# Kernel optimization log

Measured on AMD Instinct MI355X. Metric: run time of the kernel, lower is better.

Reference implementation:

```python
import jax, jax.numpy as jnp
import numpy as np

H = 51  # hidden size hardcoded in the module

def _lstm_cell(x, h, c, W_ih, W_hh, b_ih, b_hh):
    # PyTorch LSTMCell: gates ordered (i, f, g, o)
    z = x @ W_ih.T + h @ W_hh.T + b_ih + b_hh  # [B, 4H]
    i, f, g, o = jnp.split(z, 4, axis=-1)
    i = jax.nn.sigmoid(i)
    f = jax.nn.sigmoid(f)
    g = jnp.tanh(g)
    o = jax.nn.sigmoid(o)
    c_new = f * c + i * g
    h_new = o * jnp.tanh(c_new)
    return h_new, c_new

def setup_inputs() -> dict:
    key = jax.random.key(0)
    ks = jax.random.split(key, 12)
    B, T = 512, 512
    s = 1.0 / np.sqrt(H)  # PyTorch default init scale
    def u(k, shape):
        return jax.random.uniform(k, shape, jnp.float32, -s, s)
    return {
        "input": jax.random.normal(ks[0], (B, T), jnp.float32),
        "W_ih1": u(ks[1], (4 * H, 1)),
        "W_hh1": u(ks[2], (4 * H, H)),
        "b_ih1": u(ks[3], (4 * H,)),
        "b_hh1": u(ks[4], (4 * H,)),
        "W_ih2": u(ks[5], (4 * H, H)),
        "W_hh2": u(ks[6], (4 * H, H)),
        "b_ih2": u(ks[7], (4 * H,)),
        "b_hh2": u(ks[8], (4 * H,)),
        "W_lin": u(ks[9], (1, H)),
        "b_lin": u(ks[10], (1,)),
        "future": 0,
    }

def reference(input, W_ih1, W_hh1, b_ih1, b_hh1, W_ih2, W_hh2, b_ih2, b_hh2, W_lin, b_lin, future):
    B, T = input.shape
    h1 = jnp.zeros((B, H), input.dtype)
    c1 = jnp.zeros((B, H), input.dtype)
    h2 = jnp.zeros((B, H), input.dtype)
    c2 = jnp.zeros((B, H), input.dtype)

    def step(carry, x_t):
        h1, c1, h2, c2 = carry
        h1, c1 = _lstm_cell(x_t, h1, c1, W_ih1, W_hh1, b_ih1, b_hh1)
        h2, c2 = _lstm_cell(h1, h2, c2, W_ih2, W_hh2, b_ih2, b_hh2)
        out = h2 @ W_lin.T + b_lin  # [B, 1]
        return (h1, c1, h2, c2), out

    xs = jnp.transpose(input)[:, :, None]  # [T, B, 1]
    carry, outs = jax.lax.scan(step, (h1, c1, h2, c2), xs)
    outputs = jnp.transpose(outs[:, :, 0])  # [B, T]

    if future > 0:
        last = outs[-1]  # [B, 1]

        def fstep(carry, _):
            state, x = carry
            state, out = step(state, x)
            return (state, out), out

        _, fouts = jax.lax.scan(fstep, (carry, last), None, length=future)
        outputs = jnp.concatenate([outputs, jnp.transpose(fouts[:, :, 0])], axis=1)
    return outputs
```

## Files before the change

kernel.cpp:

```cpp
#include <hip/hip_runtime.h>

#define Hh 51
#define TT 512
#define MR 2
#define NBLK 256
#define BT 512
#define SHR 80
#define NIT 514
#define LOG2E 1.4426950408889634f

typedef _Float16 half8 __attribute__((ext_vector_type(8)));
typedef __attribute__((ext_vector_type(4))) float f32x4;

__device__ __forceinline__ float fexp2(float x){ return __builtin_amdgcn_exp2f(x); }
__device__ __forceinline__ float frcp(float x){ return __builtin_amdgcn_rcpf(x); }
__device__ __forceinline__ unsigned short h16bits(_Float16 h){
    union { _Float16 h; unsigned short u; } c; c.h = h; return c.u;
}
__device__ __forceinline__ unsigned packhl(float v){
    _Float16 hi = (_Float16)v;
    _Float16 lo = (_Float16)(v - (float)hi);
    return (unsigned)h16bits(hi) | ((unsigned)h16bits(lo) << 16);
}

__device__ __forceinline__ float lstm_update(float vg0, float vg1, float vg2,
                                             float vg3, float& cst){
    float ei = fexp2(vg0), ef = fexp2(vg1), eg = fexp2(vg2), eo = fexp2(vg3);
    float ii = frcp(1.f + ei);
    float ff = frcp(1.f + ef);
    float gg = fmaf(-2.f, frcp(1.f + eg), 1.f);
    float oo = frcp(1.f + eo);
    cst = fmaf(ff, cst, ii * gg);
    float r  = frcp(1.f + fexp2(2.f * LOG2E * cst));
    return fmaf(-2.f * oo, r, oo);
}

#define MFMAH(a,b,c) __builtin_amdgcn_mfma_f32_16x16x32_f16(a,b,c,0,0,0)

__global__ __launch_bounds__(BT, 2) void lstm2_fold(
    const float* __restrict__ input,
    const float* __restrict__ W_ih1,
    const float* __restrict__ W_hh1,
    const float* __restrict__ b_ih1,
    const float* __restrict__ b_hh1,
    const float* __restrict__ W_ih2,
    const float* __restrict__ W_hh2,
    const float* __restrict__ b_ih2,
    const float* __restrict__ b_hh2,
    const float* __restrict__ W_lin,
    const float* __restrict__ b_lin,
    float* __restrict__ out)
{
    __shared__ unsigned xsp[(TT+1)*MR];
    __shared__ float ob[TT*MR];
    __shared__ __align__(16) _Float16 H1[2][16*SHR];
    __shared__ __align__(16) _Float16 H2[2][16*SHR];

    const int tid  = threadIdx.x;
    const int wv   = tid >> 6;
    const int lane = tid & 63;
    const int quad = lane >> 4;
    const int n16  = lane & 15;
    const int row0 = blockIdx.x * MR;
    const bool g1  = (wv < 4);
    const bool w3  = (wv == 3);
    const int  w   = g1 ? wv : (wv - 4);
    const int  l   = 13 * w + n16;
    const bool valid = (n16 <= 12) && (l < Hh);
    const bool liveA = ((n16 & 11) == 0);
    const bool updL  = (quad < MR) && valid;
    const bool xw    = (wv == 0) && (n16 == 0) && (quad < MR);
    const int  fo    = n16 * SHR + quad * 8;
    const int  ho    = (quad * 4) * SHR + l;

#pragma unroll
    for (int i = 0; i < MR; ++i) {
        int idx = i * BT + tid; int m = idx >> 9, t = idx & 511;
        xsp[t * MR + m] = packhl(input[(row0 + m) * TT + t]);
    }
    if (tid < MR) xsp[TT * MR + tid] = 0u;
    for (int i = tid; i < 2 * 16 * SHR / 2; i += BT) {
        ((int*)H1)[i] = 0; ((int*)H2)[i] = 0;
    }

    half8 z8 = {0,0,0,0,0,0,0,0};
    half8 B1[4][2];
    half8 B2[4][2], B3[4][2];
    half8 Bout[2];
    const f32x4 zc = (f32x4){0.f,0.f,0.f,0.f};
#pragma unroll
    for (int gt = 0; gt < 4; ++gt) {
        const float gs = (gt == 2) ? (2.f * LOG2E) : (-LOG2E);
        int jrow = gt * Hh + l;
        float bias = 0.f, wih = 0.f;
        if (valid) {
            bias = gs * (g1 ? (b_ih1[jrow] + b_hh1[jrow]) : (b_ih2[jrow] + b_hh2[jrow]));
            wih  = g1 ? (gs * W_ih1[jrow]) : 0.f;
        }
        _Float16 bhi = (_Float16)bias;
        _Float16 blo = (_Float16)(bias - (float)bhi);
        _Float16 wih_h = (_Float16)wih;
#pragma unroll
        for (int kt = 0; kt < 2; ++kt) {
            B1[gt][kt] = z8; B2[gt][kt] = z8; B3[gt][kt] = z8;
#pragma unroll
            for (int jj = 0; jj < 8; ++jj) {
                int k = kt * 32 + quad * 8 + jj;
                if (valid) {
                    if (g1) {
                        if (k < Hh)       B1[gt][kt][jj] = (_Float16)(gs * W_hh1[jrow * Hh + k]);
                        else if (k == 51) B1[gt][kt][jj] = bhi;
                        else if (k == 52 || k == 53) B1[gt][kt][jj] = wih_h;
                        else if (k == 54) B1[gt][kt][jj] = blo;
                    } else {
                        if (k < Hh) {
                            B2[gt][kt][jj] = (_Float16)(gs * W_ih2[jrow * Hh + k]);
                            B3[gt][kt][jj] = (_Float16)(gs * W_hh2[jrow * Hh + k]);
                        } else if (k == 51) B2[gt][kt][jj] = bhi;
                        else if (k == 54)   B2[gt][kt][jj] = blo;
                    }
                }
            }
        }
    }
    {
        float blf = b_lin[0];
        _Float16 blhi = (_Float16)blf;
        _Float16 bllo = (_Float16)(blf - (float)blhi);
#pragma unroll
        for (int kt = 0; kt < 2; ++kt) {
            Bout[kt] = z8;
#pragma unroll
            for (int jj = 0; jj < 8; ++jj) {
                int k = kt * 32 + quad * 8 + jj;
                if (w3 && n16 == 0) {
                    if (k < Hh)       Bout[kt][jj] = (_Float16)W_lin[k];
                    else if (k == 51) Bout[kt][jj] = blhi;
                    else if (k == 54) Bout[kt][jj] = bllo;
                }
            }
        }
    }
    float cst = 0.f;

    half8 f1a = z8, f1b = z8;
    half8 f2a = z8, f2b = z8;

    __syncthreads();
    if (tid < MR) {
        int r = tid * 4 * SHR;
#pragma unroll
        for (int p = 0; p < 2; ++p) {
            H1[p][r + 51] = (_Float16)1.0f;  H1[p][r + 54] = (_Float16)1.0f;
            H2[p][r + 51] = (_Float16)1.0f;  H2[p][r + 54] = (_Float16)1.0f;
        }
        *(unsigned*)&H1[1][r + 52] = xsp[tid];
    }
    __syncthreads();

    auto stepfn = [&](int n, int pA, int pB) {
        if (g1) {
            if (w3 && n >= 2) {
                if (liveA) {
                    f2a = *(const half8*)&H2[pB][fo];
                    f2b = *(const half8*)&H2[pB][fo + 32];
                }
            }
            if (n < TT) {
                unsigned xn = xw ? xsp[(n + 1) * MR + quad] : 0u;
                if (liveA) {
                    f1a = *(const half8*)&H1[pA][fo];
                    f1b = *(const half8*)&H1[pA][fo + 32];
                }
                f32x4 ac[4];
#pragma unroll
                for (int gt = 0; gt < 4; ++gt) {
                    f32x4 a = MFMAH(f1a, B1[gt][0], zc);
                    a       = MFMAH(f1b, B1[gt][1], a);
                    ac[gt] = a;
                }
                if (updL) {
                    float h = lstm_update(ac[0][0], ac[1][0], ac[2][0], ac[3][0], cst);
                    H1[pB][ho] = (_Float16)h;
                }
                if (xw) *(unsigned*)&H1[pB][(quad * 4) * SHR + 52] = xn;
            }
            if (w3 && n >= 2) {
                f32x4 ao = MFMAH(f2a, Bout[0], zc);
                ao       = MFMAH(f2b, Bout[1], ao);
                if (n16 == 0 && quad < MR) ob[(n - 2) * MR + quad] = ao[0];
            }
        } else if (n >= 1 && n <= TT) {
            if (liveA) {
                f2a = *(const half8*)&H2[pB][fo];
                f2b = *(const half8*)&H2[pB][fo + 32];
                f1a = *(const half8*)&H1[pA][fo];
                f1b = *(const half8*)&H1[pA][fo + 32];
            }
            float vg[4];
#pragma unroll
            for (int gt = 0; gt < 4; ++gt) {
                f32x4 m2 = MFMAH(f2a, B3[gt][0], zc);
                m2       = MFMAH(f2b, B3[gt][1], m2);
                f32x4 m1 = MFMAH(f1a, B2[gt][0], zc);
                m1       = MFMAH(f1b, B2[gt][1], m1);
                vg[gt] = m2[0] + m1[0];
            }
            if (updL) {
                float h = lstm_update(vg[0], vg[1], vg[2], vg[3], cst);
                H2[pA][ho] = (_Float16)h;
            }
        }
        __syncthreads();
    };

    for (int k2 = 0; k2 < NIT / 2; ++k2) {
        stepfn(2 * k2,     1, 0);
        stepfn(2 * k2 + 1, 0, 1);
    }

#pragma unroll
    for (int i = 0; i < MR; ++i) {
        int idx = i * BT + tid; int m = idx >> 9, t = idx & 511;
        out[(row0 + m) * TT + t] = ob[t * MR + m];
    }
}

extern "C" void kernel_launch(void* const* d_in, const int* in_sizes, int n_in,
                              void* d_out, int out_size, void* d_ws, size_t ws_size,
                              hipStream_t stream) {
    const float* input = (const float*)d_in[0];
    const float* W_ih1 = (const float*)d_in[1];
    const float* W_hh1 = (const float*)d_in[2];
    const float* b_ih1 = (const float*)d_in[3];
    const float* b_hh1 = (const float*)d_in[4];
    const float* W_ih2 = (const float*)d_in[5];
    const float* W_hh2 = (const float*)d_in[6];
    const float* b_ih2 = (const float*)d_in[7];
    const float* b_hh2 = (const float*)d_in[8];
    const float* W_lin = (const float*)d_in[9];
    const float* b_lin = (const float*)d_in[10];
    float* out = (float*)d_out;

    hipLaunchKernelGGL(lstm2_fold, dim3(NBLK), dim3(BT), 0, stream,
                       input, W_ih1, W_hh1, b_ih1, b_hh1,
                       W_ih2, W_hh2, b_ih2, b_hh2, W_lin, b_lin, out);
}
```

Baseline: 268.6 us.

## Deepen layer-2 and output pipeline with register-carried prefetched fragments

Restructures the two-layer LSTM software pipeline so layer 2 consumes an h1 fragment read one step earlier and held in registers. The output projection likewise uses h2 fragments loaded one step earlier, so the pipeline is one stage longer and the iteration count grows by two. The aim is to take the LDS read latency off the per-step critical path before the MFMAs and to balance work between the two wave groups. The cost is two extra iterations, extra registers for the double-buffered fragments, and more complex index bookkeeping.

```diff
diff --git a/kernel.cpp b/kernel.cpp
--- a/kernel.cpp
+++ b/kernel.cpp
@@ -6,7 +6,7 @@
 #define NBLK 256
 #define BT 512
 #define SHR 80
-#define NIT 514
+#define NIT 516
 #define LOG2E 1.4426950408889634f
 
 typedef _Float16 half8 __attribute__((ext_vector_type(8)));
@@ -145,6 +145,8 @@
 
     half8 f1a = z8, f1b = z8;
     half8 f2a = z8, f2b = z8;
+    half8 pfA0 = z8, pfA1 = z8, pfB0 = z8, pfB1 = z8;
+    half8 ofA0 = z8, ofA1 = z8, ofB0 = z8, ofB1 = z8;
 
     __syncthreads();
     if (tid < MR) {
@@ -158,20 +160,25 @@
     }
     __syncthreads();
 
-    auto stepfn = [&](int n, int pA, int pB) {
+    auto stepfn = [&](int n, int pA, int pB,
+                      half8& pfc0, half8& pfc1, half8& pfn0, half8& pfn1,
+                      half8& ofc0, half8& ofc1, half8& ofn0, half8& ofn1) {
         if (g1) {
-            if (w3 && n >= 2) {
-                if (liveA) {
-                    f2a = *(const half8*)&H2[pB][fo];
-                    f2b = *(const half8*)&H2[pB][fo + 32];
-                }
+            if (n < TT && liveA) {
+                f1a = *(const half8*)&H1[pA][fo];
+                f1b = *(const half8*)&H1[pA][fo + 32];
+            }
+            if (w3 && liveA) {
+                ofn0 = *(const half8*)&H2[pA][fo];
+                ofn1 = *(const half8*)&H2[pA][fo + 32];
+            }
+            if (w3 && n >= 4) {
+                f32x4 ao = MFMAH(ofc0, Bout[0], zc);
+                ao       = MFMAH(ofc1, Bout[1], ao);
+                if (n16 == 0 && quad < MR) ob[(n - 4) * MR + quad] = ao[0];
             }
             if (n < TT) {
                 unsigned xn = xw ? xsp[(n + 1) * MR + quad] : 0u;
-                if (liveA) {
-                    f1a = *(const half8*)&H1[pA][fo];
-                    f1b = *(const half8*)&H1[pA][fo + 32];
-                }
                 f32x4 ac[4];
 #pragma unroll
                 for (int gt = 0; gt < 4; ++gt) {
@@ -185,38 +192,41 @@
                 }
                 if (xw) *(unsigned*)&H1[pB][(quad * 4) * SHR + 52] = xn;
             }
-            if (w3 && n >= 2) {
-                f32x4 ao = MFMAH(f2a, Bout[0], zc);
-                ao       = MFMAH(f2b, Bout[1], ao);
-                if (n16 == 0 && quad < MR) ob[(n - 2) * MR + quad] = ao[0];
-            }
-        } else if (n >= 1 && n <= TT) {
+        } else {
             if (liveA) {
-                f2a = *(const half8*)&H2[pB][fo];
-                f2b = *(const half8*)&H2[pB][fo + 32];
-                f1a = *(const half8*)&H1[pA][fo];
-                f1b = *(const half8*)&H1[pA][fo + 32];
-            }
-            float vg[4];
-#pragma unroll
-            for (int gt = 0; gt < 4; ++gt) {
-                f32x4 m2 = MFMAH(f2a, B3[gt][0], zc);
-                m2       = MFMAH(f2b, B3[gt][1], m2);
-                f32x4 m1 = MFMAH(f1a, B2[gt][0], zc);
-                m1       = MFMAH(f1b, B2[gt][1], m1);
-                vg[gt] = m2[0] + m1[0];
-            }
-            if (updL) {
-                float h = lstm_update(vg[0], vg[1], vg[2], vg[3], cst);
-                H2[pA][ho] = (_Float16)h;
+                f2a = *(const half8*)&H2[pA][fo];
+                f2b = *(const half8*)&H2[pA][fo + 32];
+                pfn0 = *(const half8*)&H1[pA][fo];
+                pfn1 = *(const half8*)&H1[pA][fo + 32];
+            }
+            if (n >= 2 && n <= TT + 1) {
+                f32x4 mih[4];
+#pragma unroll
+                for (int gt = 0; gt < 4; ++gt) {
+                    f32x4 a = MFMAH(pfc0, B2[gt][0], zc);
+                    mih[gt] = MFMAH(pfc1, B2[gt][1], a);
+                }
+                f32x4 mhh[4];
+#pragma unroll
+                for (int gt = 0; gt < 4; ++gt) {
+                    f32x4 a = MFMAH(f2a, B3[gt][0], zc);
+                    mhh[gt] = MFMAH(f2b, B3[gt][1], a);
+                }
+                float vg[4];
+#pragma unroll
+                for (int gt = 0; gt < 4; ++gt) vg[gt] = mih[gt][0] + mhh[gt][0];
+                if (updL) {
+                    float h = lstm_update(vg[0], vg[1], vg[2], vg[3], cst);
+                    H2[pB][ho] = (_Float16)h;
+                }
             }
         }
         __syncthreads();
     };
 
     for (int k2 = 0; k2 < NIT / 2; ++k2) {
-        stepfn(2 * k2,     1, 0);
-        stepfn(2 * k2 + 1, 0, 1);
+        stepfn(2 * k2,     1, 0, pfA0, pfA1, pfB0, pfB1, ofA0, ofA1, ofB0, ofB1);
+        stepfn(2 * k2 + 1, 0, 1, pfB0, pfB1, pfA0, pfA1, ofB0, ofB1, ofA0, ofA1);
     }
 
 #pragma unroll
```

Result: no change. 272.2 us (+1.3%).
